# Kernel tuning notes

Measured on AMD Instinct MI355X. Metric: run time of the kernel, lower is better.

## Reference

```python
import jax, jax.numpy as jnp
import numpy as np

T, B, D, H = 256, 128, 128, 1024
MEL = 48           # preprocess.melodyRange
MELODY_COEFF = 0.5
FORGET_BIAS = 1.0  # TF BasicLSTMCell default


def setup_inputs() -> dict:
    key = jax.random.key(0)
    ks = jax.random.split(key, 8)
    s = 0.05
    return {
        "inSeq": jax.random.normal(ks[0], (T, B, D), dtype=jnp.float32),
        "targetSeq": jax.random.randint(ks[1], (T, B, 2), 0, MEL).astype(jnp.int64),
        "W1": jax.random.normal(ks[2], (D + H, 4 * H), dtype=jnp.float32) * s,
        "b1": jnp.zeros((4 * H,), dtype=jnp.float32),
        "W2": jax.random.normal(ks[3], (2 * H, 4 * H), dtype=jnp.float32) * s,
        "b2": jnp.zeros((4 * H,), dtype=jnp.float32),
        "outW": jax.random.normal(ks[4], (H, D), dtype=jnp.float32) * s,
        "outB": jnp.zeros((D,), dtype=jnp.float32),
    }


def _lstm_cell(x, c, h, W, b):
    # TF BasicLSTMCell: gates in (i, j, f, o) order, forget_bias added to f
    z = jnp.concatenate([x, h], axis=-1) @ W + b
    i, j, f, o = jnp.split(z, 4, axis=-1)
    c_new = c * jax.nn.sigmoid(f + FORGET_BIAS) + jax.nn.sigmoid(i) * jnp.tanh(j)
    h_new = jnp.tanh(c_new) * jax.nn.sigmoid(o)
    return c_new, h_new


def _forward(inSeq, targetSeq, W1, b1, W2, b2, outW, outB):
    dt = inSeq.dtype
    zero = jnp.zeros((B, H), dtype=dt)

    def step(carry, x):
        c1, h1, c2, h2 = carry
        c1, h1 = _lstm_cell(x, c1, h1, W1, b1)
        c2, h2 = _lstm_cell(h1, c2, h2, W2, b2)
        return (c1, h1, c2, h2), h2

    _, outputs = jax.lax.scan(step, (zero, zero, zero, zero), inSeq)  # [T,B,H]
    logits = outputs @ outW + outB                                    # [T,B,D]

    mel_logits = logits[..., :MEL]
    har_logits = logits[..., MEL:]

    # probs: per-timestep dual softmax, concatenated
    probs = jnp.concatenate(
        [jax.nn.softmax(mel_logits, axis=-1), jax.nn.softmax(har_logits, axis=-1)],
        axis=-1,
    )

    # dual sparse softmax cross-entropy
    mel_lp = jax.nn.log_softmax(mel_logits, axis=-1)
    har_lp = jax.nn.log_softmax(har_logits, axis=-1)
    mel_ce = -jnp.take_along_axis(mel_lp, targetSeq[..., 0:1], axis=-1)[..., 0]
    har_ce = -jnp.take_along_axis(har_lp, targetSeq[..., 1:2], axis=-1)[..., 0]
    losses = MELODY_COEFF * mel_ce + (1.0 - MELODY_COEFF) * har_ce
    loss = jnp.sum(losses) / T / B
    return probs, loss


def reference(inSeq, targetSeq, W1, b1, W2, b2, outW, outB):
    return _forward(inSeq, targetSeq, W1, b1, W2, b2, outW, outB)
```

## Files before the change

### kernel.cpp

```cpp
#include <hip/hip_runtime.h>
#include <cstdint>
#include <cstddef>

#define T_ 256
#define B_ 128
#define D_ 128
#define H_ 1024
#define K1_ 1152
#define K2_ 2048

#define R_ 32
#define SOFF 64
#define FS 64

typedef __bf16 bf16x8 __attribute__((ext_vector_type(8)));
typedef short s8 __attribute__((ext_vector_type(8)));
typedef float f32x4 __attribute__((ext_vector_type(4)));

__device__ __forceinline__ unsigned short f2bf(float f) {
  unsigned int u = __builtin_bit_cast(unsigned int, f);
  u += 0x7fff + ((u >> 16) & 1);
  return (unsigned short)(u >> 16);
}
__device__ __forceinline__ float sigm(float x) { return 1.f / (1.f + __expf(-x)); }
__device__ __forceinline__ float tanh_(float x) { return 1.f - 2.f / (__expf(2.f * x) + 1.f); }

__device__ __forceinline__ f32x4 mfma16(s8 a, s8 b, f32x4 c) {
  return __builtin_amdgcn_mfma_f32_16x16x32_bf16(
      __builtin_bit_cast(bf16x8, a), __builtin_bit_cast(bf16x8, b), c, 0, 0, 0);
}

__device__ __forceinline__ void wait_ge(int* p, int want) {
  while (__hip_atomic_load(p, __ATOMIC_RELAXED, __HIP_MEMORY_SCOPE_AGENT) < want)
    __builtin_amdgcn_s_sleep(2);
}

__device__ __forceinline__ void st_bypass_short(unsigned short* p, unsigned int v) {
  asm volatile("global_store_short %0, %1, off sc0 sc1" :: "v"(p), "v"(v) : "memory");
}

__global__ void prep_misc(const float* __restrict__ inSeq,
                          const float* __restrict__ outW,
                          unsigned short* __restrict__ xbf,
                          unsigned short* __restrict__ outWp,
                          unsigned short* __restrict__ h1b,
                          unsigned short* __restrict__ h1r,
                          unsigned short* __restrict__ h2all,
                          float* __restrict__ c1, float* __restrict__ c2,
                          float* __restrict__ loss,
                          int* __restrict__ s1, int* __restrict__ s2)
{
  int i = blockIdx.x * 256 + threadIdx.x;
  if (i < T_ * B_ * D_) xbf[i] = f2bf(inSeq[i]);
  if (i < B_ * H_) {
    c1[i] = 0.f; c2[i] = 0.f;
    h1b[B_ * H_ + i] = 0;
    if (h1r) h1r[(size_t)(R_ - 1) * B_ * H_ + i] = 0;
    h2all[i] = 0;
  }
  if (i < H_ * D_) {
    int c = i >> 10, k = i & 1023;
    outWp[i] = f2bf(outW[(size_t)k * D_ + c]);
  }
  if (s1 && i < T_ + SOFF) {
    s1[(size_t)i * FS] = (i < SOFF) ? 256 : 0;
    s2[(size_t)i * FS] = (i < SOFF) ? 256 : 0;
  }
  if (i == 0) loss[0] = 0.f;
}

__global__ void pack_w(const float* __restrict__ src, unsigned short* __restrict__ dst, int K)
{
  __shared__ float tile[64][65];
  int k0 = blockIdx.x * 64, j0 = blockIdx.y * 64, g = blockIdx.z;
  int tid = threadIdx.x;
#pragma unroll
  for (int e = 0; e < 16; ++e) {
    int li = e * 256 + tid;
    int kl = li >> 6, jl = li & 63;
    tile[kl][jl] = src[(size_t)(k0 + kl) * 4096 + g * 1024 + j0 + jl];
  }
  __syncthreads();
#pragma unroll
  for (int e = 0; e < 16; ++e) {
    int li = e * 256 + tid;
    int jl = li >> 6, kl = li & 63;
    dst[(size_t)((j0 + jl) * 4 + g) * K + k0 + kl] = f2bf(tile[kl][jl]);
  }
}

__global__ __launch_bounds__(256, 2) void phase_kernel(
    int p,
    const unsigned short* __restrict__ xbf,
    const unsigned short* __restrict__ W1p,
    const unsigned short* __restrict__ W2p,
    const float* __restrict__ b1,
    const float* __restrict__ b2,
    unsigned short* __restrict__ h1b,
    unsigned short* __restrict__ h2all,
    float* __restrict__ c1,
    float* __restrict__ c2)
{
  __shared__ float red[4][2048];
  const int bid = blockIdx.x;
  const bool isL2 = bid >= 256;
  if (!isL2 && p >= T_) return;
  if (isL2 && p == 0) return;
  const int jb = isL2 ? (bid - 256) : bid;
  const int mt = jb & 1, nt = jb >> 1;
  const int t = isL2 ? (p - 1) : p;
  const int r0 = mt * 64, c0 = nt * 32;
  const int tid = threadIdx.x;
  const int wid = tid >> 6, lane = tid & 63;
  const int quad = lane >> 4, l15 = lane & 15;
  const int kseg = quad * 8;

  const unsigned short* hsrc = h1b + (size_t)((p + 1) & 1) * (B_ * H_);

  f32x4 acc[4][2];
#pragma unroll
  for (int i = 0; i < 4; ++i)
#pragma unroll
    for (int j = 0; j < 2; ++j) acc[i][j] = (f32x4){0.f, 0.f, 0.f, 0.f};

  int arow[4], bcol[2];
#pragma unroll
  for (int i = 0; i < 4; ++i) arow[i] = r0 + i * 16 + l15;
#pragma unroll
  for (int j = 0; j < 2; ++j) bcol[j] = c0 + j * 16 + l15;

  if (!isL2) {
    const unsigned short* xt = xbf + (size_t)t * (B_ * D_);
    const int cpw = 9;
    const int kcbase = wid * cpw;
    s8 a[4], b[2], an[4], bn[2];
    auto LD = [&](int kc, s8* A, s8* Bv) {
      int kk = kc * 32 + kseg;
      if (kk < D_) {
#pragma unroll
        for (int i = 0; i < 4; ++i) A[i] = *(const s8*)(xt + (size_t)arow[i] * D_ + kk);
      } else {
#pragma unroll
        for (int i = 0; i < 4; ++i) A[i] = *(const s8*)(hsrc + (size_t)arow[i] * H_ + (kk - D_));
      }
#pragma unroll
      for (int j = 0; j < 2; ++j) Bv[j] = *(const s8*)(W1p + (size_t)bcol[j] * K1_ + kk);
    };
    LD(kcbase, a, b);
    for (int c = 0; c < cpw; ++c) {
      if (c + 1 < cpw) LD(kcbase + c + 1, an, bn);
#pragma unroll
      for (int i = 0; i < 4; ++i)
#pragma unroll
        for (int j = 0; j < 2; ++j) acc[i][j] = mfma16(a[i], b[j], acc[i][j]);
#pragma unroll
      for (int i = 0; i < 4; ++i) a[i] = an[i];
      b[0] = bn[0]; b[1] = bn[1];
    }
  } else {
    const unsigned short* h2prev = h2all + (size_t)t * (B_ * H_);
    const int cpw = 16;
    const int kcbase = wid * cpw;
    s8 a[4], b[2], an[4], bn[2];
    auto LD = [&](int kc, s8* A, s8* Bv) {
      int kk = kc * 32 + kseg;
      if (kk < H_) {
#pragma unroll
        for (int i = 0; i < 4; ++i) A[i] = *(const s8*)(hsrc + (size_t)arow[i] * H_ + kk);
      } else {
#pragma unroll
        for (int i = 0; i < 4; ++i) A[i] = *(const s8*)(h2prev + (size_t)arow[i] * H_ + (kk - H_));
      }
#pragma unroll
      for (int j = 0; j < 2; ++j) Bv[j] = *(const s8*)(W2p + (size_t)bcol[j] * K2_ + kk);
    };
    LD(kcbase, a, b);
    for (int c = 0; c < cpw; ++c) {
      if (c + 1 < cpw) LD(kcbase + c + 1, an, bn);
#pragma unroll
      for (int i = 0; i < 4; ++i)
#pragma unroll
        for (int j = 0; j < 2; ++j) acc[i][j] = mfma16(a[i], b[j], acc[i][j]);
#pragma unroll
      for (int i = 0; i < 4; ++i) a[i] = an[i];
      b[0] = bn[0]; b[1] = bn[1];
    }
  }

#pragma unroll
  for (int i = 0; i < 4; ++i)
#pragma unroll
    for (int j = 0; j < 2; ++j)
#pragma unroll
      for (int r = 0; r < 4; ++r)
        red[wid][(i * 16 + quad * 4 + r) * 32 + (j * 16 + l15)] = acc[i][j][r];
  __syncthreads();
#pragma unroll
  for (int it = 0; it < 8; ++it) {
    int e = it * 256 + tid;
    red[0][e] = red[0][e] + red[1][e] + red[2][e] + red[3][e];
  }
  __syncthreads();

  const float* bias = isL2 ? b2 : b1;
  float* cst = isL2 ? c2 : c1;
  unsigned short* hout = isL2 ? (h2all + (size_t)(t + 1) * (B_ * H_))
                              : (h1b + (size_t)(p & 1) * (B_ * H_));
#pragma unroll
  for (int it = 0; it < 2; ++it) {
    int s = it * 256 + tid;
    int row = s >> 3, u = s & 7;
    int jg = (c0 >> 2) + u;
    float zi = red[0][row * 32 + u * 4 + 0] + bias[0 * H_ + jg];
    float zj = red[0][row * 32 + u * 4 + 1] + bias[1 * H_ + jg];
    float zf = red[0][row * 32 + u * 4 + 2] + bias[2 * H_ + jg];
    float zo = red[0][row * 32 + u * 4 + 3] + bias[3 * H_ + jg];
    int rg = r0 + row;
    float co = cst[(size_t)rg * H_ + jg];
    float cn = co * sigm(zf + 1.0f) + sigm(zi) * tanh_(zj);
    float hn = tanh_(cn) * sigm(zo);
    cst[(size_t)rg * H_ + jg] = cn;
    hout[(size_t)rg * H_ + jg] = f2bf(hn);
  }
}

__global__ __launch_bounds__(256, 2) void lstm_persistent(
    const unsigned short* __restrict__ xbf,
    const unsigned short* __restrict__ W1p,
    const unsigned short* __restrict__ W2p,
    const float* __restrict__ b1,
    const float* __restrict__ b2,
    unsigned short* __restrict__ h1r,
    unsigned short* __restrict__ h2all,
    int* __restrict__ s1,
    int* __restrict__ s2)
{
  __shared__ float red[4][2048];
  const int bid = blockIdx.x;
  const bool isL2 = bid >= 256;
  const int jb = isL2 ? (bid - 256) : bid;
  const int mt = jb & 1, nt = jb >> 1;
  const int r0 = mt * 64, c0 = nt * 32;
  const int tid = threadIdx.x;
  const int wid = tid >> 6, lane = tid & 63;
  const int quad = lane >> 4, l15 = lane & 15;
  const int kseg = quad * 8;

  int arow[4], bcol[2];
#pragma unroll
  for (int i = 0; i < 4; ++i) arow[i] = r0 + i * 16 + l15;
#pragma unroll
  for (int j = 0; j < 2; ++j) bcol[j] = c0 + j * 16 + l15;

  const float* bias = isL2 ? b2 : b1;
  int ridx[2];
  unsigned hoff[2];
  float bz[2][4], creg[2];
#pragma unroll
  for (int it = 0; it < 2; ++it) {
    int s = it * 256 + tid;
    int row = s >> 3, u = s & 7;
    int jg = (c0 >> 2) + u;
    ridx[it] = row * 32 + u * 4;
    hoff[it] = (unsigned)((r0 + row) * H_ + jg);
#pragma unroll
    for (int g = 0; g < 4; ++g) bz[it][g] = bias[g * H_ + jg];
    creg[it] = 0.f;
  }

  if (!isL2) {
    const int kcbase = wid * 9;
    s8 bw[9][2];
#pragma unroll
    for (int c = 0; c < 9; ++c) {
      int kk = (kcbase + c) * 32 + kseg;
      bw[c][0] = *(const s8*)(W1p + (size_t)bcol[0] * K1_ + kk);
      bw[c][1] = *(const s8*)(W1p + (size_t)bcol[1] * K1_ + kk);
    }
#pragma unroll
    for (int c = 0; c < 9; ++c)
      asm volatile("" : "+v"(bw[c][0]), "+v"(bw[c][1]));

    for (int t = 0; t < T_; ++t) {
      if (tid == 0) {
        wait_ge(s1 + (size_t)(t - 1 + SOFF) * FS, 256);
        wait_ge(s2 + (size_t)(t - R_ + SOFF) * FS, 256);
      }
      __syncthreads();
      if ((t & (R_ - 1)) == 0 && t)
        __builtin_amdgcn_fence(__ATOMIC_ACQUIRE, "agent");
      asm volatile("" ::: "memory");

      const unsigned short* hsrc = h1r + (size_t)((t + R_ - 1) & (R_ - 1)) * (B_ * H_);
      const unsigned short* xt = xbf + (size_t)t * (B_ * D_);
      f32x4 acc[4][2];
#pragma unroll
      for (int i = 0; i < 4; ++i)
#pragma unroll
        for (int j = 0; j < 2; ++j) acc[i][j] = (f32x4){0.f, 0.f, 0.f, 0.f};
      s8 a[4], an[4];
      auto LD = [&](int kc, s8* A) {
        int kk = kc * 32 + kseg;
        if (kk < D_) {
#pragma unroll
          for (int i = 0; i < 4; ++i) A[i] = *(const s8*)(xt + (size_t)arow[i] * D_ + kk);
        } else {
#pragma unroll
          for (int i = 0; i < 4; ++i) A[i] = *(const s8*)(hsrc + (size_t)arow[i] * H_ + (kk - D_));
        }
      };
      LD(kcbase, a);
#pragma unroll
      for (int c = 0; c < 9; ++c) {
        if (c + 1 < 9) LD(kcbase + c + 1, an);
#pragma unroll
        for (int i = 0; i < 4; ++i)
#pragma unroll
          for (int j = 0; j < 2; ++j) acc[i][j] = mfma16(a[i], bw[c][j], acc[i][j]);
#pragma unroll
        for (int i = 0; i < 4; ++i) a[i] = an[i];
      }
#pragma unroll
      for (int i = 0; i < 4; ++i)
#pragma unroll
        for (int j = 0; j < 2; ++j)
#pragma unroll
          for (int r = 0; r < 4; ++r)
            red[wid][(i * 16 + quad * 4 + r) * 32 + (j * 16 + l15)] = acc[i][j][r];
      __syncthreads();
#pragma unroll
      for (int it = 0; it < 8; ++it) {
        int e = it * 256 + tid;
        red[0][e] = red[0][e] + red[1][e] + red[2][e] + red[3][e];
      }
      __syncthreads();
      unsigned short* hout = h1r + (size_t)(t & (R_ - 1)) * (B_ * H_);
#pragma unroll
      for (int it = 0; it < 2; ++it) {
        float zi = red[0][ridx[it] + 0] + bz[it][0];
        float zj = red[0][ridx[it] + 1] + bz[it][1];
        float zf = red[0][ridx[it] + 2] + bz[it][2];
        float zo = red[0][ridx[it] + 3] + bz[it][3];
        float cn = creg[it] * sigm(zf + 1.0f) + sigm(zi) * tanh_(zj);
        float hn = tanh_(cn) * sigm(zo);
        creg[it] = cn;
        st_bypass_short(hout + hoff[it], (unsigned int)f2bf(hn));
      }
      asm volatile("s_waitcnt vmcnt(0)" ::: "memory");
      __syncthreads();
      if (tid == 0)
        __hip_atomic_fetch_add(s1 + (size_t)(t + SOFF) * FS, 1, __ATOMIC_RELAXED,
                               __HIP_MEMORY_SCOPE_AGENT);
    }
  } else {
    const int kcbase = wid * 16;
    s8 bw[16][2];
#pragma unroll
    for (int c = 0; c < 16; ++c) {
      int kk = (kcbase + c) * 32 + kseg;
      bw[c][0] = *(const s8*)(W2p + (size_t)bcol[0] * K2_ + kk);
      bw[c][1] = *(const s8*)(W2p + (size_t)bcol[1] * K2_ + kk);
    }
#pragma unroll
    for (int c = 0; c < 16; ++c)
      asm volatile("" : "+v"(bw[c][0]), "+v"(bw[c][1]));

    for (int t = 0; t < T_; ++t) {
      if (tid == 0) {
        wait_ge(s1 + (size_t)(t + SOFF) * FS, 256);
        wait_ge(s2 + (size_t)(t - 1 + SOFF) * FS, 256);
      }
      __syncthreads();
      if ((t & (R_ - 1)) == 0 && t)
        __builtin_amdgcn_fence(__ATOMIC_ACQUIRE, "agent");
      asm volatile("" ::: "memory");

      const unsigned short* hsrc = h1r + (size_t)(t & (R_ - 1)) * (B_ * H_);
      const unsigned short* h2prev = h2all + (size_t)t * (B_ * H_);
      f32x4 acc[4][2];
#pragma unroll
      for (int i = 0; i < 4; ++i)
#pragma unroll
        for (int j = 0; j < 2; ++j) acc[i][j] = (f32x4){0.f, 0.f, 0.f, 0.f};
      s8 a[4], an[4];
      auto LD = [&](int kc, s8* A) {
        int kk = kc * 32 + kseg;
        if (kk < H_) {
#pragma unroll
          for (int i = 0; i < 4; ++i) A[i] = *(const s8*)(hsrc + (size_t)arow[i] * H_ + kk);
        } else {
#pragma unroll
          for (int i = 0; i < 4; ++i) A[i] = *(const s8*)(h2prev + (size_t)arow[i] * H_ + (kk - H_));
        }
      };
      LD(kcbase, a);
#pragma unroll
      for (int c = 0; c < 16; ++c) {
        if (c + 1 < 16) LD(kcbase + c + 1, an);
#pragma unroll
        for (int i = 0; i < 4; ++i)
#pragma unroll
          for (int j = 0; j < 2; ++j) acc[i][j] = mfma16(a[i], bw[c][j], acc[i][j]);
#pragma unroll
        for (int i = 0; i < 4; ++i) a[i] = an[i];
      }
#pragma unroll
      for (int i = 0; i < 4; ++i)
#pragma unroll
        for (int j = 0; j < 2; ++j)
#pragma unroll
          for (int r = 0; r < 4; ++r)
            red[wid][(i * 16 + quad * 4 + r) * 32 + (j * 16 + l15)] = acc[i][j][r];
      __syncthreads();
#pragma unroll
      for (int it = 0; it < 8; ++it) {
        int e = it * 256 + tid;
        red[0][e] = red[0][e] + red[1][e] + red[2][e] + red[3][e];
      }
      __syncthreads();
      unsigned short* hout = h2all + (size_t)(t + 1) * (B_ * H_);
#pragma unroll
      for (int it = 0; it < 2; ++it) {
        float zi = red[0][ridx[it] + 0] + bz[it][0];
        float zj = red[0][ridx[it] + 1] + bz[it][1];
        float zf = red[0][ridx[it] + 2] + bz[it][2];
        float zo = red[0][ridx[it] + 3] + bz[it][3];
        float cn = creg[it] * sigm(zf + 1.0f) + sigm(zi) * tanh_(zj);
        float hn = tanh_(cn) * sigm(zo);
        creg[it] = cn;
        st_bypass_short(hout + hoff[it], (unsigned int)f2bf(hn));
      }
      asm volatile("s_waitcnt vmcnt(0)" ::: "memory");
      __syncthreads();
      if (tid == 0)
        __hip_atomic_fetch_add(s2 + (size_t)(t + SOFF) * FS, 1, __ATOMIC_RELAXED,
                               __HIP_MEMORY_SCOPE_AGENT);
    }
  }
}

__global__ __launch_bounds__(256, 1) void proj_kernel(
    const unsigned short* __restrict__ h2flat,
    const unsigned short* __restrict__ outWp,
    const float* __restrict__ outB,
    const int* __restrict__ targets,
    float* __restrict__ out,
    float* __restrict__ loss)
{
  __shared__ float lg[128][129];
  __shared__ float red2[256];
  const int r0 = blockIdx.x * 128;
  const int tid = threadIdx.x;
  const int wid = tid >> 6, lane = tid & 63;
  const int quad = lane >> 4, l15 = lane & 15;
  const int wr = (wid & 1) * 64, wc = (wid >> 1) * 64;
  const int kseg = quad * 8;

  f32x4 acc[4][4];
#pragma unroll
  for (int i = 0; i < 4; ++i)
#pragma unroll
    for (int j = 0; j < 4; ++j) acc[i][j] = (f32x4){0.f, 0.f, 0.f, 0.f};

  int arow[4], bcolv[4];
#pragma unroll
  for (int i = 0; i < 4; ++i) arow[i] = r0 + wr + i * 16 + l15;
#pragma unroll
  for (int j = 0; j < 4; ++j) bcolv[j] = wc + j * 16 + l15;

  s8 a[4], b[4], an[4], bn[4];
  auto LD = [&](int kc, s8* A, s8* Bv) {
    int kk = kc * 32 + kseg;
#pragma unroll
    for (int i = 0; i < 4; ++i) A[i] = *(const s8*)(h2flat + (size_t)arow[i] * H_ + kk);
#pragma unroll
    for (int j = 0; j < 4; ++j) Bv[j] = *(const s8*)(outWp + (size_t)bcolv[j] * H_ + kk);
  };
  LD(0, a, b);
  for (int c = 0; c < 32; ++c) {
    if (c + 1 < 32) LD(c + 1, an, bn);
#pragma unroll
    for (int i = 0; i < 4; ++i)
#pragma unroll
      for (int j = 0; j < 4; ++j) acc[i][j] = mfma16(a[i], b[j], acc[i][j]);
#pragma unroll
    for (int i = 0; i < 4; ++i) a[i] = an[i];
#pragma unroll
    for (int j = 0; j < 4; ++j) b[j] = bn[j];
  }

#pragma unroll
  for (int i = 0; i < 4; ++i)
#pragma unroll
    for (int j = 0; j < 4; ++j)
#pragma unroll
      for (int r = 0; r < 4; ++r)
        lg[wr + i * 16 + quad * 4 + r][wc + j * 16 + l15] = acc[i][j][r] + outB[bcolv[j]];
  __syncthreads();

  const int row = tid >> 1, half = tid & 1;
  const int cbeg = half ? 48 : 0, cend = half ? 128 : 48;
  float m = -1e30f;
  for (int c = cbeg; c < cend; ++c) m = fmaxf(m, lg[row][c]);
  float s = 0.f;
  for (int c = cbeg; c < cend; ++c) s += __expf(lg[row][c] - m);
  float rinv = 1.f / s;
  float* orow = out + (size_t)(r0 + row) * D_;
  for (int c = cbeg; c < cend; ++c) orow[c] = __expf(lg[row][c] - m) * rinv;

  int tg = targets[(size_t)(r0 + row) * 2 + half];
  int tc = half ? (48 + tg) : tg;
  float ce = -(lg[row][tc] - m - logf(s));
  red2[tid] = 0.5f * ce;
  __syncthreads();
  for (int o = 128; o > 0; o >>= 1) {
    if (tid < o) red2[tid] += red2[tid + o];
    __syncthreads();
  }
  if (tid == 0) atomicAdd(loss, red2[0]);
}

__global__ void finalize_loss(const float* __restrict__ loss, float* __restrict__ out)
{
  out[(size_t)T_ * B_ * D_] = loss[0] * (1.f / (float)(T_ * B_));
}

extern "C" void kernel_launch(void* const* d_in, const int* in_sizes, int n_in,
                              void* d_out, int out_size, void* d_ws, size_t ws_size,
                              hipStream_t stream)
{
  const float* inSeq = (const float*)d_in[0];
  const int* targets = (const int*)d_in[1];
  const float* W1 = (const float*)d_in[2];
  const float* b1 = (const float*)d_in[3];
  const float* W2 = (const float*)d_in[4];
  const float* b2 = (const float*)d_in[5];
  const float* outW = (const float*)d_in[6];
  const float* outB = (const float*)d_in[7];
  float* out = (float*)d_out;

  char* w = (char*)d_ws;
  auto alloc = [&](size_t bytes) {
    char* r = w;
    w += (bytes + 255) & ~(size_t)255;
    return r;
  };
  unsigned short* W1p = (unsigned short*)alloc((size_t)4096 * K1_ * 2);
  unsigned short* W2p = (unsigned short*)alloc((size_t)4096 * K2_ * 2);
  unsigned short* xbf = (unsigned short*)alloc((size_t)T_ * B_ * D_ * 2);
  unsigned short* h1b = (unsigned short*)alloc((size_t)2 * B_ * H_ * 2);
  unsigned short* h2all = (unsigned short*)alloc((size_t)(T_ + 1) * B_ * H_ * 2);
  float* c1 = (float*)alloc((size_t)B_ * H_ * 4);
  float* c2 = (float*)alloc((size_t)B_ * H_ * 4);
  unsigned short* outWp = (unsigned short*)alloc((size_t)H_ * D_ * 2);
  float* loss = (float*)alloc(256);
  int* s1 = (int*)alloc((size_t)(T_ + SOFF) * FS * 4);
  int* s2 = (int*)alloc((size_t)(T_ + SOFF) * FS * 4);
  unsigned short* h1r = (unsigned short*)alloc((size_t)R_ * B_ * H_ * 2);

  const bool fits = ((size_t)(w - (char*)d_ws) <= ws_size);
  if (!fits) { s1 = nullptr; s2 = nullptr; h1r = nullptr; }

  prep_misc<<<dim3((T_ * B_ * D_) / 256), dim3(256), 0, stream>>>(
      inSeq, outW, xbf, outWp, h1b, h1r, h2all, c1, c2, loss, s1, s2);
  pack_w<<<dim3(K1_ / 64, 16, 4), dim3(256), 0, stream>>>(W1, W1p, K1_);
  pack_w<<<dim3(K2_ / 64, 16, 4), dim3(256), 0, stream>>>(W2, W2p, K2_);

  hipError_t ce = hipErrorUnknown;
  if (fits) {
    void* kargs[] = {(void*)&xbf, (void*)&W1p, (void*)&W2p, (void*)&b1,
                     (void*)&b2,  (void*)&h1r, (void*)&h2all,
                     (void*)&s1,  (void*)&s2};
    ce = hipLaunchCooperativeKernel((const void*)lstm_persistent,
                                    dim3(512), dim3(256), kargs, 0, stream);
  }
  if (ce != hipSuccess) {
    (void)hipGetLastError();
    for (int p = 0; p <= T_; ++p)
      phase_kernel<<<dim3(512), dim3(256), 0, stream>>>(
          p, xbf, W1p, W2p, b1, b2, h1b, h2all, c1, c2);
  }

  proj_kernel<<<dim3(256), dim3(256), 0, stream>>>(
      h2all + (size_t)B_ * H_, outWp, outB, targets, out, loss);
  finalize_loss<<<dim3(1), dim3(1), 0, stream>>>(loss, out);
}
```

Measured before the change: 5.985 ms.

## Replace atomic step counters with per-block flags polled by every wave

Cross-block step signalling changes from atomic increments on a shared counter per timestep to each block storing its own step number into a flag array. Each wave polls all 256 flags with vector loads and a wave-wide vote, and layer-2 waves wait only on the layer whose state they read. This removes atomic contention and the block-wide barrier after the wait, so it should shorten the per-step critical path. In exchange, every wave issues more polling traffic each step.

```diff
diff --git a/kernel.cpp b/kernel.cpp
--- a/kernel.cpp
+++ b/kernel.cpp
@@ -10,8 +10,6 @@
 #define K2_ 2048
 
 #define R_ 32
-#define SOFF 64
-#define FS 64
 
 typedef __bf16 bf16x8 __attribute__((ext_vector_type(8)));
 typedef short s8 __attribute__((ext_vector_type(8)));
@@ -30,13 +28,36 @@
       __builtin_bit_cast(bf16x8, a), __builtin_bit_cast(bf16x8, b), c, 0, 0, 0);
 }
 
-__device__ __forceinline__ void wait_ge(int* p, int want) {
-  while (__hip_atomic_load(p, __ATOMIC_RELAXED, __HIP_MEMORY_SCOPE_AGENT) < want)
-    __builtin_amdgcn_s_sleep(2);
-}
-
 __device__ __forceinline__ void st_bypass_short(unsigned short* p, unsigned int v) {
   asm volatile("global_store_short %0, %1, off sc0 sc1" :: "v"(p), "v"(v) : "memory");
+}
+__device__ __forceinline__ void st_flag(int* p, int v) {
+  asm volatile("global_store_dword %0, %1, off sc0 sc1" :: "v"(p), "v"(v) : "memory");
+}
+
+__device__ __forceinline__ void wave_wait1(const int* p, int want) {
+  for (;;) {
+    int4 v;
+    asm volatile("global_load_dwordx4 %0, %1, off sc0 sc1\n\ts_waitcnt vmcnt(0)"
+                 : "=v"(v) : "v"(p) : "memory");
+    int ok = (v.x >= want) && (v.y >= want) && (v.z >= want) && (v.w >= want);
+    if (__all(ok)) break;
+    __builtin_amdgcn_s_sleep(1);
+  }
+}
+__device__ __forceinline__ void wave_wait2(const int* pa, int wa,
+                                           const int* pb, int wb) {
+  for (;;) {
+    int4 a, b;
+    asm volatile("global_load_dwordx4 %0, %2, off sc0 sc1\n\t"
+                 "global_load_dwordx4 %1, %3, off sc0 sc1\n\t"
+                 "s_waitcnt vmcnt(0)"
+                 : "=v"(a), "=v"(b) : "v"(pa), "v"(pb) : "memory");
+    int ok = (a.x >= wa) && (a.y >= wa) && (a.z >= wa) && (a.w >= wa) &&
+             (b.x >= wb) && (b.y >= wb) && (b.z >= wb) && (b.w >= wb);
+    if (__all(ok)) break;
+    __builtin_amdgcn_s_sleep(1);
+  }
 }
 
 __global__ void prep_misc(const float* __restrict__ inSeq,
@@ -48,7 +69,7 @@
                           unsigned short* __restrict__ h2all,
                           float* __restrict__ c1, float* __restrict__ c2,
                           float* __restrict__ loss,
-                          int* __restrict__ s1, int* __restrict__ s2)
+                          int* __restrict__ f1, int* __restrict__ f2)
 {
   int i = blockIdx.x * 256 + threadIdx.x;
   if (i < T_ * B_ * D_) xbf[i] = f2bf(inSeq[i]);
@@ -62,10 +83,7 @@
     int c = i >> 10, k = i & 1023;
     outWp[i] = f2bf(outW[(size_t)k * D_ + c]);
   }
-  if (s1 && i < T_ + SOFF) {
-    s1[(size_t)i * FS] = (i < SOFF) ? 256 : 0;
-    s2[(size_t)i * FS] = (i < SOFF) ? 256 : 0;
-  }
+  if (f1 && i < 256) { f1[i] = 0; f2[i] = 0; }
   if (i == 0) loss[0] = 0.f;
 }
 
@@ -232,8 +250,8 @@
     const float* __restrict__ b2,
     unsigned short* __restrict__ h1r,
     unsigned short* __restrict__ h2all,
-    int* __restrict__ s1,
-    int* __restrict__ s2)
+    int* __restrict__ f1,
+    int* __restrict__ f2)
 {
   __shared__ float red[4][2048];
   const int bid = blockIdx.x;
@@ -245,6 +263,7 @@
   const int wid = tid >> 6, lane = tid & 63;
   const int quad = lane >> 4, l15 = lane & 15;
   const int kseg = quad * 8;
+  const int lane4 = lane * 4;
 
   int arow[4], bcol[2];
 #pragma unroll
@@ -282,14 +301,9 @@
       asm volatile("" : "+v"(bw[c][0]), "+v"(bw[c][1]));
 
     for (int t = 0; t < T_; ++t) {
-      if (tid == 0) {
-        wait_ge(s1 + (size_t)(t - 1 + SOFF) * FS, 256);
-        wait_ge(s2 + (size_t)(t - R_ + SOFF) * FS, 256);
-      }
-      __syncthreads();
+      wave_wait2(f1 + lane4, t, f2 + lane4, t - (R_ - 1));
       if ((t & (R_ - 1)) == 0 && t)
         __builtin_amdgcn_fence(__ATOMIC_ACQUIRE, "agent");
-      asm volatile("" ::: "memory");
 
       const unsigned short* hsrc = h1r + (size_t)((t + R_ - 1) & (R_ - 1)) * (B_ * H_);
       const unsigned short* xt = xbf + (size_t)t * (B_ * D_);
@@ -348,9 +362,7 @@
       }
       asm volatile("s_waitcnt vmcnt(0)" ::: "memory");
       __syncthreads();
-      if (tid == 0)
-        __hip_atomic_fetch_add(s1 + (size_t)(t + SOFF) * FS, 1, __ATOMIC_RELAXED,
-                               __HIP_MEMORY_SCOPE_AGENT);
+      if (tid == 0) st_flag(f1 + bid, t + 1);
     }
   } else {
     const int kcbase = wid * 16;
@@ -366,14 +378,10 @@
       asm volatile("" : "+v"(bw[c][0]), "+v"(bw[c][1]));
 
     for (int t = 0; t < T_; ++t) {
-      if (tid == 0) {
-        wait_ge(s1 + (size_t)(t + SOFF) * FS, 256);
-        wait_ge(s2 + (size_t)(t - 1 + SOFF) * FS, 256);
-      }
-      __syncthreads();
+      if (wid < 2) wave_wait1(f1 + lane4, t + 1);
+      else         wave_wait1(f2 + lane4, t);
       if ((t & (R_ - 1)) == 0 && t)
         __builtin_amdgcn_fence(__ATOMIC_ACQUIRE, "agent");
-      asm volatile("" ::: "memory");
 
       const unsigned short* hsrc = h1r + (size_t)(t & (R_ - 1)) * (B_ * H_);
       const unsigned short* h2prev = h2all + (size_t)t * (B_ * H_);
@@ -432,9 +440,7 @@
       }
       asm volatile("s_waitcnt vmcnt(0)" ::: "memory");
       __syncthreads();
-      if (tid == 0)
-        __hip_atomic_fetch_add(s2 + (size_t)(t + SOFF) * FS, 1, __ATOMIC_RELAXED,
-                               __HIP_MEMORY_SCOPE_AGENT);
+      if (tid == 0) st_flag(f2 + bid - 256, t + 1);
     }
   }
 }
@@ -554,15 +560,15 @@
   float* c2 = (float*)alloc((size_t)B_ * H_ * 4);
   unsigned short* outWp = (unsigned short*)alloc((size_t)H_ * D_ * 2);
   float* loss = (float*)alloc(256);
-  int* s1 = (int*)alloc((size_t)(T_ + SOFF) * FS * 4);
-  int* s2 = (int*)alloc((size_t)(T_ + SOFF) * FS * 4);
+  int* f1 = (int*)alloc(256 * 4);
+  int* f2 = (int*)alloc(256 * 4);
   unsigned short* h1r = (unsigned short*)alloc((size_t)R_ * B_ * H_ * 2);
 
   const bool fits = ((size_t)(w - (char*)d_ws) <= ws_size);
-  if (!fits) { s1 = nullptr; s2 = nullptr; h1r = nullptr; }
+  if (!fits) { f1 = nullptr; f2 = nullptr; h1r = nullptr; }
 
   prep_misc<<<dim3((T_ * B_ * D_) / 256), dim3(256), 0, stream>>>(
-      inSeq, outW, xbf, outWp, h1b, h1r, h2all, c1, c2, loss, s1, s2);
+      inSeq, outW, xbf, outWp, h1b, h1r, h2all, c1, c2, loss, f1, f2);
   pack_w<<<dim3(K1_ / 64, 16, 4), dim3(256), 0, stream>>>(W1, W1p, K1_);
   pack_w<<<dim3(K2_ / 64, 16, 4), dim3(256), 0, stream>>>(W2, W2p, K2_);
 
@@ -570,7 +576,7 @@
   if (fits) {
     void* kargs[] = {(void*)&xbf, (void*)&W1p, (void*)&W2p, (void*)&b1,
                      (void*)&b2,  (void*)&h1r, (void*)&h2all,
-                     (void*)&s1,  (void*)&s2};
+                     (void*)&f1,  (void*)&f2};
     ce = hipLaunchCooperativeKernel((const void*)lstm_persistent,
                                     dim3(512), dim3(256), kargs, 0, stream);
   }
```

Result: faster. 5.515 ms (-7.9%).
